# Kernel optimization log

Measured on AMD Instinct MI355X. Metric: run time of the kernel, lower is better.

## Reference

```python
import jax, jax.numpy as jnp
import numpy as np

BLOCK_SIZE = 32
# NVFP4 decode table: index bit3 = sign, bits0-2 = magnitude code
DECODE = jnp.array([0.0, 0.5, 1.0, 1.5, 2.0, 3.0, 4.0, 6.0,
                    -0.0, -0.5, -1.0, -1.5, -2.0, -3.0, -4.0, -6.0], dtype=jnp.float32)

N_OUT, K_IN = 16384, 4096


def setup_inputs() -> dict:
    key = jax.random.key(0)
    k1, k2, k3, k4 = jax.random.split(key, 4)
    x = jax.random.normal(k1, (4, 512, K_IN), dtype=jnp.float32)
    # packed uint8 stored as int32 in [0, 256)
    weight_packed = jax.random.randint(k2, (N_OUT, K_IN // 2), 0, 256, dtype=jnp.int32)
    # per-block positive scales (block_max / 6.0 in the original)
    weight_scales = jax.random.uniform(k3, (N_OUT, K_IN // BLOCK_SIZE), dtype=jnp.float32,
                                       minval=1e-3, maxval=5e-2)
    bias = jax.random.normal(k4, (N_OUT,), dtype=jnp.float32) * 0.02
    return {"x": x, "weight_packed": weight_packed, "weight_scales": weight_scales, "bias": bias}


def _dequant(weight_packed, weight_scales):
    # unpack: low nibble -> even K index, high nibble -> odd K index
    low = DECODE[weight_packed & 15]           # [N, K//2]
    high = DECODE[(weight_packed >> 4) & 15]   # [N, K//2]
    n = weight_packed.shape[0]
    w = jnp.stack([low, high], axis=-1).reshape(n, -1)  # [N, K], interleaved
    # expand per-block scales along K
    scales = jnp.repeat(weight_scales, BLOCK_SIZE, axis=1)  # [N, K]
    return w * scales


def reference(x, weight_packed, weight_scales, bias):
    w = _dequant(weight_packed, weight_scales)            # [N, K]
    out = jnp.einsum('bsk,nk->bsn', x, w) + bias          # [B, S, N]
    # activation='gelu' -> F.gelu(approximate='tanh')
    return jax.nn.gelu(out, approximate=True)
```

## Files before the change

### kernel.cpp

```cpp
#include <hip/hip_runtime.h>
#include <hip/hip_bf16.h>

typedef short bf16x8 __attribute__((ext_vector_type(8)));
typedef float f32x4 __attribute__((ext_vector_type(4)));
typedef float f32x16 __attribute__((ext_vector_type(16)));

#define K_DIM 4096
#define N_DIM 16384
#define M_DIM 2048
#define STRIPE 16384
#define TSTRIDE (64 * STRIPE)
#define WSB_BYTES ((size_t)N_DIM * K_DIM * 2)
#define WSA_BYTES ((size_t)M_DIM * K_DIM * 2)

__device__ __forceinline__ unsigned f2bf(float f) {
    unsigned u = __builtin_bit_cast(unsigned, f);
    u += 0x7FFFu + ((u >> 16) & 1u);
    return u >> 16;
}

__device__ __forceinline__ float dec4(unsigned c, float s) {
    unsigned mag = c & 7u;
    unsigned u = (mag >= 2u) ? ((((mag >> 1) + 126u) << 23) | ((mag & 1u) << 22))
                             : (mag == 1u ? 0x3F000000u : 0u);
    u |= (c & 8u) << 28;
    return __builtin_bit_cast(float, u) * s;
}

__device__ __forceinline__ float gelu_tanh(float v) {
    float c = v + 0.044715f * v * v * v;
    float t = tanhf(0.7978845608028654f * c);
    return 0.5f * v * (1.0f + t);
}

__global__ __launch_bounds__(256) void dequant_w(const int* __restrict__ wp,
                                                 const float* __restrict__ wsc,
                                                 unsigned char* __restrict__ dst) {
    int t = blockIdx.x * 256 + threadIdx.x;
    int n = t >> 9;
    int ck = t & 511;
    int kstep = ck >> 3, s = ck & 7;
    int nt = n >> 7, r = n & 127;

    const int4 p4 = *reinterpret_cast<const int4*>(wp + (size_t)n * (K_DIM / 2) + kstep * 32 + s * 4);
    float scale = wsc[(size_t)n * (K_DIM / 32) + kstep * 2 + (s >> 2)];

    const int pv[4] = {p4.x, p4.y, p4.z, p4.w};
    unsigned o[8];
    #pragma unroll
    for (int j = 0; j < 4; ++j) {
        unsigned b = (unsigned)pv[j] & 255u;
        o[2 * j]     = f2bf(dec4(b & 15u, scale));
        o[2 * j + 1] = f2bf(dec4((b >> 4) & 15u, scale));
    }
    uint4 v;
    v.x = o[0] | (o[1] << 16);
    v.y = o[2] | (o[3] << 16);
    v.z = o[4] | (o[5] << 16);
    v.w = o[6] | (o[7] << 16);

    size_t off = (size_t)(nt * 64 + kstep) * STRIPE
               + (size_t)r * 128 + (size_t)((s ^ (r & 7)) << 4);
    *reinterpret_cast<uint4*>(dst + off) = v;
}

__global__ __launch_bounds__(256) void conv_x(const float* __restrict__ x,
                                              unsigned char* __restrict__ dst) {
    int t = blockIdx.x * 256 + threadIdx.x;
    int m = t >> 9;
    int ck = t & 511;
    int kstep = ck >> 3, s = ck & 7;
    int mt = m >> 7, r = m & 127;

    const float4* xp = reinterpret_cast<const float4*>(x + (size_t)m * K_DIM + kstep * 64 + s * 8);
    float4 a = xp[0], b = xp[1];
    uint4 v;
    v.x = f2bf(a.x) | (f2bf(a.y) << 16);
    v.y = f2bf(a.z) | (f2bf(a.w) << 16);
    v.z = f2bf(b.x) | (f2bf(b.y) << 16);
    v.w = f2bf(b.z) | (f2bf(b.w) << 16);

    size_t off = (size_t)(mt * 64 + kstep) * STRIPE
               + (size_t)r * 128 + (size_t)((s ^ (r & 7)) << 4);
    *reinterpret_cast<uint4*>(dst + off) = v;
}


__global__ __launch_bounds__(512, 2) void gemm_bf16_256(
    const unsigned char* __restrict__ wsA,
    const unsigned char* __restrict__ wsB,
    const float* __restrict__ bias,
    float* __restrict__ out)
{
    __shared__ unsigned char lds[131072];

    int id = blockIdx.x;
    int wg = (id & 7) * 64 + (id >> 3);
    int MT = wg & 7;
    int NT = wg >> 3;

    const int tid  = threadIdx.x;
    const int lane = tid & 63;
    const int w    = tid >> 6;
    const int wm   = w >> 2;
    const int wn   = w & 3;
    const int l31  = lane & 31;
    const int lh   = lane >> 5;

    const unsigned char* gA = wsA + (size_t)(2 * MT) * TSTRIDE;
    const unsigned char* gB = wsB + (size_t)(2 * NT) * TSTRIDE;

    int addrA[8];
    #pragma unroll
    for (int mi = 0; mi < 4; ++mi) {
        int row = wm * 128 + mi * 32 + l31;
        int L = row >> 1;
        #pragma unroll
        for (int kk = 0; kk < 2; ++kk) {
            int kq = kk * 2 + lh;
            addrA[mi * 2 + kk] = L * 128 + (((((row & 1) << 2) | kq) ^ (L & 7)) << 4);
        }
    }
    int addrB[4];
    #pragma unroll
    for (int bi = 0; bi < 2; ++bi) {
        int row = wn * 64 + bi * 32 + l31;
        int L = row >> 1;
        #pragma unroll
        for (int kk = 0; kk < 2; ++kk) {
            int kq = kk * 2 + lh;
            addrB[bi * 2 + kk] = L * 128 + (((((row & 1) << 2) | kq) ^ (L & 7)) << 4);
        }
    }

    int offST[2][2];
    #pragma unroll
    for (int j = 0; j < 2; ++j) {
        int c = w * 2 + j;
        int L = c * 8 + (lane >> 3);
        int p = lane & 7;
        int sl = p ^ (L & 7);
        int h = sl >> 2, fgs = sl & 3;
        int row = 2 * L + h;
        #pragma unroll
        for (int kb = 0; kb < 2; ++kb)
            offST[j][kb] = (row >> 7) * TSTRIDE + (row & 127) * 128
                         + ((((kb << 2) | fgs) ^ (row & 7)) << 4);
    }

#define GLDS(SRC, DOFF) __builtin_amdgcn_global_load_lds(                          \
        (const __attribute__((address_space(1))) unsigned int*)(SRC),              \
        (__attribute__((address_space(3))) unsigned int*)(&lds[DOFF]), 16, 0, 0)

#define STAGE_A(KSOFF, KB, SLOT) do {                                              \
        GLDS(gA + (KSOFF) + offST[0][KB], ((SLOT) << 14) + (w * 2 + 0) * 1024);    \
        GLDS(gA + (KSOFF) + offST[1][KB], ((SLOT) << 14) + (w * 2 + 1) * 1024);    \
    } while (0)
#define STAGE_B(KSOFF, KB, SLOT) do {                                              \
        GLDS(gB + (KSOFF) + offST[0][KB], 65536 + ((SLOT) << 14) + (w * 2 + 0) * 1024); \
        GLDS(gB + (KSOFF) + offST[1][KB], 65536 + ((SLOT) << 14) + (w * 2 + 1) * 1024); \
    } while (0)

    f32x16 acc[4][2];
    #pragma unroll
    for (int mi = 0; mi < 4; ++mi)
        #pragma unroll
        for (int bi = 0; bi < 2; ++bi)
            #pragma unroll
            for (int q = 0; q < 16; ++q)
                acc[mi][bi][q] = 0.f;

    STAGE_A(0, 0, 0);        STAGE_B(0, 0, 0);
    STAGE_A(0, 1, 1);        STAGE_B(0, 1, 1);
    STAGE_A(STRIPE, 0, 2);   STAGE_B(STRIPE, 0, 2);
    asm volatile("s_waitcnt vmcnt(8)" ::: "memory");
    __builtin_amdgcn_sched_barrier(0);
    __builtin_amdgcn_s_barrier();
    __builtin_amdgcn_sched_barrier(0);

#define TILE_BODY(RSLOT, DO_STG, STKS, STKB, SSLOT, VMN) do {                      \
        const unsigned char* la = lds + ((RSLOT) << 14);                           \
        const unsigned char* lb = lds + 65536 + ((RSLOT) << 14);                   \
        bf16x8 af[4], bfr[2];                                                      \
        if (DO_STG) STAGE_A(STKS, STKB, SSLOT);                                    \
        _Pragma("unroll") for (int bi = 0; bi < 2; ++bi)                           \
            bfr[bi] = *reinterpret_cast<const bf16x8*>(lb + addrB[bi * 2 + 0]);    \
        _Pragma("unroll") for (int mi = 0; mi < 4; ++mi)                           \
            af[mi] = *reinterpret_cast<const bf16x8*>(la + addrA[mi * 2 + 0]);     \
        __builtin_amdgcn_s_setprio(1);                                             \
        _Pragma("unroll") for (int mi = 0; mi < 4; ++mi)                           \
            _Pragma("unroll") for (int bi = 0; bi < 2; ++bi)                       \
                acc[mi][bi] = __builtin_amdgcn_mfma_f32_32x32x16_bf16(             \
                    af[mi], bfr[bi], acc[mi][bi], 0, 0, 0);                        \
        __builtin_amdgcn_s_setprio(0);                                             \
        if (DO_STG) STAGE_B(STKS, STKB, SSLOT);                                    \
        _Pragma("unroll") for (int bi = 0; bi < 2; ++bi)                           \
            bfr[bi] = *reinterpret_cast<const bf16x8*>(lb + addrB[bi * 2 + 1]);    \
        _Pragma("unroll") for (int mi = 0; mi < 4; ++mi)                           \
            af[mi] = *reinterpret_cast<const bf16x8*>(la + addrA[mi * 2 + 1]);     \
        __builtin_amdgcn_s_setprio(1);                                             \
        _Pragma("unroll") for (int mi = 0; mi < 4; ++mi)                           \
            _Pragma("unroll") for (int bi = 0; bi < 2; ++bi)                       \
                acc[mi][bi] = __builtin_amdgcn_mfma_f32_32x32x16_bf16(             \
                    af[mi], bfr[bi], acc[mi][bi], 0, 0, 0);                        \
        __builtin_amdgcn_s_setprio(0);                                             \
        if ((VMN) >= 0) {                                                          \
            if ((VMN) == 8)      asm volatile("s_waitcnt vmcnt(8)" ::: "memory");  \
            else if ((VMN) == 4) asm volatile("s_waitcnt vmcnt(4)" ::: "memory");  \
            else                 asm volatile("s_waitcnt vmcnt(0)" ::: "memory");  \
            __builtin_amdgcn_sched_barrier(0);                                     \
            __builtin_amdgcn_s_barrier();                                          \
            __builtin_amdgcn_sched_barrier(0);                                     \
        }                                                                          \
    } while (0)

    for (int tp = 0; tp < 62; ++tp) {
        const int scur = (tp & 1) << 1;
        const int ks1 = (tp + 1) * STRIPE;
        const int ks2 = (tp + 2) * STRIPE;
        TILE_BODY(scur,     1, ks1, 1, scur ^ 3, 8);
        TILE_BODY(scur ^ 1, 1, ks2, 0, scur,     8);
    }
    TILE_BODY(0, 1, 63 * STRIPE, 1, 3, 8);
    TILE_BODY(1, 0, 0, 0, 0, 4);
    TILE_BODY(2, 0, 0, 0, 0, 0);
    TILE_BODY(3, 0, 0, 0, 0, -1);

    const int bm0 = MT * 256, bn0 = NT * 256;
    #pragma unroll
    for (int mi = 0; mi < 4; ++mi) {
        int rbase = bm0 + wm * 128 + mi * 32 + lh * 4;
        #pragma unroll
        for (int bi = 0; bi < 2; ++bi) {
            int col = bn0 + wn * 64 + bi * 32 + l31;
            float bv = bias[col];
            #pragma unroll
            for (int reg = 0; reg < 16; ++reg) {
                int row = rbase + (reg & 3) + 8 * (reg >> 2);
                float v = acc[mi][bi][reg] + bv;
                out[(size_t)row * N_DIM + col] = gelu_tanh(v);
            }
        }
    }
#undef TILE_BODY
#undef STAGE_A
#undef STAGE_B
#undef GLDS
}

__global__ __launch_bounds__(256, 2) void nvfp4_gemm(
    const float* __restrict__ x,
    const int*   __restrict__ wp,
    const float* __restrict__ wscale,
    const float* __restrict__ bias,
    float* __restrict__ out)
{
    __shared__ uint4  lsA[128 * 8];
    __shared__ uint4  lsB[128 * 8];
    __shared__ float2 lut[256];

    const int tid = threadIdx.x;
    {
        static const float dectab[16] = {0.f, 0.5f, 1.f, 1.5f, 2.f, 3.f, 4.f, 6.f,
                                         -0.f,-0.5f,-1.f,-1.5f,-2.f,-3.f,-4.f,-6.f};
        lut[tid] = make_float2(dectab[tid & 15], dectab[(tid >> 4) & 15]);
    }

    const int bn0 = blockIdx.x * 128;
    const int bm0 = blockIdx.y * 128;
    const int r = tid >> 1;
    const int h = tid & 1;

    const float4* xp = reinterpret_cast<const float4*>(x + (size_t)(bm0 + r) * K_DIM) + h * 8;
    const uint4*  bp = reinterpret_cast<const uint4*>(wp + (size_t)(bn0 + r) * (K_DIM / 2)) + h * 4;
    const float*  sp = wscale + (size_t)(bn0 + r) * (K_DIM / 32) + h;

    float4 ax[8];
    uint4  bx[4];
    float  scale;
    #pragma unroll
    for (int j = 0; j < 8; ++j) ax[j] = xp[j];
    #pragma unroll
    for (int q = 0; q < 4; ++q) bx[q] = bp[q];
    scale = sp[0];

    f32x4 acc[4][4];
    #pragma unroll
    for (int mi = 0; mi < 4; ++mi)
        #pragma unroll
        for (int ni = 0; ni < 4; ++ni)
            acc[mi][ni] = (f32x4){0.f, 0.f, 0.f, 0.f};

    const int lane = tid & 63;
    const int wid  = tid >> 6;
    const int wm0  = (wid >> 1) * 64;
    const int wn0  = (wid & 1) * 64;
    const int fr   = lane & 15;
    const int fg   = lane >> 4;

    __syncthreads();

    for (int kt = 0; kt < 64; ++kt) {
        #pragma unroll
        for (int j = 0; j < 4; ++j) {
            float4 f0 = ax[2 * j], f1 = ax[2 * j + 1];
            uint4 v;
            v.x = f2bf(f0.x) | (f2bf(f0.y) << 16);
            v.y = f2bf(f0.z) | (f2bf(f0.w) << 16);
            v.z = f2bf(f1.x) | (f2bf(f1.y) << 16);
            v.w = f2bf(f1.z) | (f2bf(f1.w) << 16);
            lsA[(r * 8 + h * 4 + j) ^ (r & 7)] = v;
        }
        #pragma unroll
        for (int q = 0; q < 4; ++q) {
            uint4 p = bx[q];
            float2 d0 = lut[p.x & 255];
            float2 d1 = lut[p.y & 255];
            float2 d2 = lut[p.z & 255];
            float2 d3 = lut[p.w & 255];
            uint4 v;
            v.x = f2bf(d0.x * scale) | (f2bf(d0.y * scale) << 16);
            v.y = f2bf(d1.x * scale) | (f2bf(d1.y * scale) << 16);
            v.z = f2bf(d2.x * scale) | (f2bf(d2.y * scale) << 16);
            v.w = f2bf(d3.x * scale) | (f2bf(d3.y * scale) << 16);
            lsB[(r * 8 + h * 4 + q) ^ (r & 7)] = v;
        }
        __syncthreads();

        if (kt + 1 < 64) {
            #pragma unroll
            for (int j = 0; j < 8; ++j) ax[j] = xp[(kt + 1) * 16 + j];
            #pragma unroll
            for (int q = 0; q < 4; ++q) bx[q] = bp[(kt + 1) * 8 + q];
            scale = sp[(kt + 1) * 2];
        }

        #pragma unroll
        for (int kk = 0; kk < 2; ++kk) {
            bf16x8 af[4], bfr[4];
            #pragma unroll
            for (int mi = 0; mi < 4; ++mi) {
                int row = wm0 + mi * 16 + fr;
                af[mi] = __builtin_bit_cast(bf16x8, lsA[(row * 8 + kk * 4 + fg) ^ (row & 7)]);
            }
            #pragma unroll
            for (int ni = 0; ni < 4; ++ni) {
                int row = wn0 + ni * 16 + fr;
                bfr[ni] = __builtin_bit_cast(bf16x8, lsB[(row * 8 + kk * 4 + fg) ^ (row & 7)]);
            }
            #pragma unroll
            for (int mi = 0; mi < 4; ++mi)
                #pragma unroll
                for (int ni = 0; ni < 4; ++ni)
                    acc[mi][ni] = __builtin_amdgcn_mfma_f32_16x16x32_bf16(
                        af[mi], bfr[ni], acc[mi][ni], 0, 0, 0);
        }
        __syncthreads();
    }

    #pragma unroll
    for (int mi = 0; mi < 4; ++mi) {
        int row = bm0 + wm0 + mi * 16 + fg * 4;
        #pragma unroll
        for (int ni = 0; ni < 4; ++ni) {
            int col = bn0 + wn0 + ni * 16 + fr;
            float bv = bias[col];
            float* op = out + (size_t)row * N_DIM + col;
            #pragma unroll
            for (int q = 0; q < 4; ++q) {
                float v = acc[mi][ni][q] + bv;
                op[(size_t)q * N_DIM] = gelu_tanh(v);
            }
        }
    }
}

extern "C" void kernel_launch(void* const* d_in, const int* in_sizes, int n_in,
                              void* d_out, int out_size, void* d_ws, size_t ws_size,
                              hipStream_t stream) {
    const float* x    = (const float*)d_in[0];
    const int*   wp   = (const int*)d_in[1];
    const float* wsc  = (const float*)d_in[2];
    const float* bias = (const float*)d_in[3];
    float*       out  = (float*)d_out;
    (void)in_sizes; (void)n_in; (void)out_size;

    if (ws_size >= WSB_BYTES + WSA_BYTES) {
        unsigned char* wsB = (unsigned char*)d_ws;
        unsigned char* wsA = wsB + WSB_BYTES;
        dequant_w<<<(N_DIM * (K_DIM / 8)) / 256, 256, 0, stream>>>(wp, wsc, wsB);
        conv_x<<<(M_DIM * (K_DIM / 8)) / 256, 256, 0, stream>>>(x, wsA);
        gemm_bf16_256<<<(M_DIM / 256) * (N_DIM / 256), 512, 0, stream>>>(wsA, wsB, bias, out);
    } else {
        dim3 grid(N_DIM / 128, M_DIM / 128);
        nvfp4_gemm<<<grid, 256, 0, stream>>>(x, wp, wsc, bias, out);
    }
}
```

Measured before the change: 340.3 us.

## Prefetch next tile's first LDS fragments and change LDS fragment layout

Restructures the bf16 GEMM main loop so the first k-half fragments of the next LDS slot are read during the current tile's second MFMA batch, with double-buffered register fragments. It also changes the staging and read address mapping to a new swizzled LDS layout, and tightens vmcnt waits so the next slot is resident before it is prefetched. The aim is to hide LDS read latency behind MFMAs, at the cost of more VGPRs and a stricter wait on outstanding global loads.

New measurement: 335.6 us. No clear change (-1.4%).

```diff
diff --git a/kernel.cpp b/kernel.cpp
--- a/kernel.cpp
+++ b/kernel.cpp
@@ -110,42 +110,31 @@
     const unsigned char* gA = wsA + (size_t)(2 * MT) * TSTRIDE;
     const unsigned char* gB = wsB + (size_t)(2 * NT) * TSTRIDE;
 
-    int addrA[8];
-    #pragma unroll
-    for (int mi = 0; mi < 4; ++mi) {
-        int row = wm * 128 + mi * 32 + l31;
-        int L = row >> 1;
-        #pragma unroll
-        for (int kk = 0; kk < 2; ++kk) {
-            int kq = kk * 2 + lh;
-            addrA[mi * 2 + kk] = L * 128 + (((((row & 1) << 2) | kq) ^ (L & 7)) << 4);
-        }
-    }
-    int addrB[4];
-    #pragma unroll
-    for (int bi = 0; bi < 2; ++bi) {
-        int row = wn * 64 + bi * 32 + l31;
-        int L = row >> 1;
-        #pragma unroll
-        for (int kk = 0; kk < 2; ++kk) {
-            int kq = kk * 2 + lh;
-            addrB[bi * 2 + kk] = L * 128 + (((((row & 1) << 2) | kq) ^ (L & 7)) << 4);
-        }
-    }
+    int addrA[4][2];
+    #pragma unroll
+    for (int mi = 0; mi < 4; ++mi)
+        #pragma unroll
+        for (int kk = 0; kk < 2; ++kk)
+            addrA[mi][kk] = (wm * 16 + mi * 4 + (l31 >> 3)) * 512
+                          + (kk * 2 + lh) * 128 + (l31 & 7) * 16;
+    int addrB[2][2];
+    #pragma unroll
+    for (int bi = 0; bi < 2; ++bi)
+        #pragma unroll
+        for (int kk = 0; kk < 2; ++kk)
+            addrB[bi][kk] = (wn * 8 + bi * 4 + (l31 >> 3)) * 512
+                          + (kk * 2 + lh) * 128 + (l31 & 7) * 16;
 
     int offST[2][2];
     #pragma unroll
     for (int j = 0; j < 2; ++j) {
         int c = w * 2 + j;
-        int L = c * 8 + (lane >> 3);
-        int p = lane & 7;
-        int sl = p ^ (L & 7);
-        int h = sl >> 2, fgs = sl & 3;
-        int row = 2 * L + h;
+        int row = c * 16 + (lane >> 5) * 8 + (lane & 7);
+        int kq = (lane >> 3) & 3;
         #pragma unroll
         for (int kb = 0; kb < 2; ++kb)
             offST[j][kb] = (row >> 7) * TSTRIDE + (row & 127) * 128
-                         + ((((kb << 2) | fgs) ^ (row & 7)) << 4);
+                         + ((((kb << 2) | kq) ^ (row & 7)) << 4);
     }
 
 #define GLDS(SRC, DOFF) __builtin_amdgcn_global_load_lds(                          \
@@ -161,6 +150,15 @@
         GLDS(gB + (KSOFF) + offST[1][KB], 65536 + ((SLOT) << 14) + (w * 2 + 1) * 1024); \
     } while (0)
 
+#define READ_PF(PA, PB, SLOT) do {                                                 \
+        const unsigned char* La_ = lds + ((SLOT) << 14);                           \
+        const unsigned char* Lb_ = lds + 65536 + ((SLOT) << 14);                   \
+        _Pragma("unroll") for (int bi = 0; bi < 2; ++bi)                           \
+            PB[bi] = *reinterpret_cast<const bf16x8*>(Lb_ + addrB[bi][0]);         \
+        _Pragma("unroll") for (int mi = 0; mi < 4; ++mi)                           \
+            PA[mi] = *reinterpret_cast<const bf16x8*>(La_ + addrA[mi][0]);         \
+    } while (0)
+
     f32x16 acc[4][2];
     #pragma unroll
     for (int mi = 0; mi < 4; ++mi)
@@ -169,44 +167,43 @@
             #pragma unroll
             for (int q = 0; q < 16; ++q)
                 acc[mi][bi][q] = 0.f;
+
+    bf16x8 pa0[4], pb0[2], pa1[4], pb1[2];
 
     STAGE_A(0, 0, 0);        STAGE_B(0, 0, 0);
     STAGE_A(0, 1, 1);        STAGE_B(0, 1, 1);
     STAGE_A(STRIPE, 0, 2);   STAGE_B(STRIPE, 0, 2);
-    asm volatile("s_waitcnt vmcnt(8)" ::: "memory");
+    asm volatile("s_waitcnt vmcnt(4)" ::: "memory");
     __builtin_amdgcn_sched_barrier(0);
     __builtin_amdgcn_s_barrier();
     __builtin_amdgcn_sched_barrier(0);
-
-#define TILE_BODY(RSLOT, DO_STG, STKS, STKB, SSLOT, VMN) do {                      \
+    READ_PF(pa0, pb0, 0);
+
+#define TILE_BODY(RSLOT, NSLOT, PA, PB, NPA, NPB, DO_STG, STKS, STKB, SSLOT, DO_PF, VMN) do { \
         const unsigned char* la = lds + ((RSLOT) << 14);                           \
         const unsigned char* lb = lds + 65536 + ((RSLOT) << 14);                   \
-        bf16x8 af[4], bfr[2];                                                      \
+        bf16x8 ka[4], kb2[2];                                                      \
         if (DO_STG) STAGE_A(STKS, STKB, SSLOT);                                    \
         _Pragma("unroll") for (int bi = 0; bi < 2; ++bi)                           \
-            bfr[bi] = *reinterpret_cast<const bf16x8*>(lb + addrB[bi * 2 + 0]);    \
+            kb2[bi] = *reinterpret_cast<const bf16x8*>(lb + addrB[bi][1]);         \
         _Pragma("unroll") for (int mi = 0; mi < 4; ++mi)                           \
-            af[mi] = *reinterpret_cast<const bf16x8*>(la + addrA[mi * 2 + 0]);     \
+            ka[mi] = *reinterpret_cast<const bf16x8*>(la + addrA[mi][1]);          \
         __builtin_amdgcn_s_setprio(1);                                             \
         _Pragma("unroll") for (int mi = 0; mi < 4; ++mi)                           \
             _Pragma("unroll") for (int bi = 0; bi < 2; ++bi)                       \
                 acc[mi][bi] = __builtin_amdgcn_mfma_f32_32x32x16_bf16(             \
-                    af[mi], bfr[bi], acc[mi][bi], 0, 0, 0);                        \
+                    PA[mi], PB[bi], acc[mi][bi], 0, 0, 0);                         \
         __builtin_amdgcn_s_setprio(0);                                             \
         if (DO_STG) STAGE_B(STKS, STKB, SSLOT);                                    \
-        _Pragma("unroll") for (int bi = 0; bi < 2; ++bi)                           \
-            bfr[bi] = *reinterpret_cast<const bf16x8*>(lb + addrB[bi * 2 + 1]);    \
-        _Pragma("unroll") for (int mi = 0; mi < 4; ++mi)                           \
-            af[mi] = *reinterpret_cast<const bf16x8*>(la + addrA[mi * 2 + 1]);     \
+        if (DO_PF) READ_PF(NPA, NPB, NSLOT);                                       \
         __builtin_amdgcn_s_setprio(1);                                             \
         _Pragma("unroll") for (int mi = 0; mi < 4; ++mi)                           \
             _Pragma("unroll") for (int bi = 0; bi < 2; ++bi)                       \
                 acc[mi][bi] = __builtin_amdgcn_mfma_f32_32x32x16_bf16(             \
-                    af[mi], bfr[bi], acc[mi][bi], 0, 0, 0);                        \
+                    ka[mi], kb2[bi], acc[mi][bi], 0, 0, 0);                        \
         __builtin_amdgcn_s_setprio(0);                                             \
         if ((VMN) >= 0) {                                                          \
-            if ((VMN) == 8)      asm volatile("s_waitcnt vmcnt(8)" ::: "memory");  \
-            else if ((VMN) == 4) asm volatile("s_waitcnt vmcnt(4)" ::: "memory");  \
+            if ((VMN) == 4)      asm volatile("s_waitcnt vmcnt(4)" ::: "memory");  \
             else                 asm volatile("s_waitcnt vmcnt(0)" ::: "memory");  \
             __builtin_amdgcn_sched_barrier(0);                                     \
             __builtin_amdgcn_s_barrier();                                          \
@@ -218,13 +215,13 @@
         const int scur = (tp & 1) << 1;
         const int ks1 = (tp + 1) * STRIPE;
         const int ks2 = (tp + 2) * STRIPE;
-        TILE_BODY(scur,     1, ks1, 1, scur ^ 3, 8);
-        TILE_BODY(scur ^ 1, 1, ks2, 0, scur,     8);
-    }
-    TILE_BODY(0, 1, 63 * STRIPE, 1, 3, 8);
-    TILE_BODY(1, 0, 0, 0, 0, 4);
-    TILE_BODY(2, 0, 0, 0, 0, 0);
-    TILE_BODY(3, 0, 0, 0, 0, -1);
+        TILE_BODY(scur,     scur ^ 1, pa0, pb0, pa1, pb1, 1, ks1, 1, scur ^ 3, 1, 4);
+        TILE_BODY(scur ^ 1, scur ^ 2, pa1, pb1, pa0, pb0, 1, ks2, 0, scur,     1, 4);
+    }
+    TILE_BODY(0, 1, pa0, pb0, pa1, pb1, 1, 63 * STRIPE, 1, 3, 1, 4);
+    TILE_BODY(1, 2, pa1, pb1, pa0, pb0, 0, 0, 0, 0, 1, 0);
+    TILE_BODY(2, 3, pa0, pb0, pa1, pb1, 0, 0, 0, 0, 1, 0);
+    TILE_BODY(3, 0, pa1, pb1, pa0, pb0, 0, 0, 0, 0, 0, -1);
 
     const int bm0 = MT * 256, bn0 = NT * 256;
     #pragma unroll
@@ -243,6 +240,7 @@
         }
     }
 #undef TILE_BODY
+#undef READ_PF
 #undef STAGE_A
 #undef STAGE_B
 #undef GLDS
```
